# Performance work log

Measured on AMD Instinct MI355X. Metric: run time of the kernel, lower is better.

Reference implementation:

```python
import jax, jax.numpy as jnp
import numpy as np

N_NODES = 100000


def setup_inputs() -> dict:
    key = jax.random.key(0)
    ks = jax.random.split(key, 9)
    E = 1600000
    x = jax.random.normal(ks[0], (N_NODES, 12), dtype=jnp.float32)
    edge_index = jax.random.randint(ks[1], (2, E), 0, N_NODES, dtype=jnp.int64)
    def glorot(k, shape):
        lim = float(np.sqrt(6.0 / (shape[0] + shape[1])))
        return jax.random.uniform(k, shape, jnp.float32, -lim, lim)
    return {
        "x": x,
        "edge_index": edge_index,
        "W1": glorot(ks[2], (12, 64)),
        "b1": jnp.zeros((64,), jnp.float32),
        "W2": glorot(ks[3], (64, 128)),
        "b2": jnp.zeros((128,), jnp.float32),
        "W3": glorot(ks[4], (128, 96)),
        "b3": jnp.zeros((96,), jnp.float32),
    }


def reference(x, edge_index, W1, b1, W2, b2, W3, b3):
    N = x.shape[0]
    F_channel, n_his = 8, 12
    src, dst = edge_index[0], edge_index[1]
    # add self loops (PyG GCNConv default)
    loop = jnp.arange(N, dtype=src.dtype)
    src = jnp.concatenate([src, loop])
    dst = jnp.concatenate([dst, loop])
    # symmetric normalization: norm_e = deg[src]^-1/2 * deg[dst]^-1/2
    deg = jax.ops.segment_sum(jnp.ones_like(src, dtype=x.dtype), dst, num_segments=N)
    dinv = jnp.where(deg > 0, jax.lax.rsqrt(deg), 0.0)
    norm = dinv[src] * dinv[dst]  # [E+N]

    def gcn(h, W, b):
        hw = h @ W  # transform first (out_ch <= in-edge fanout cost)
        agg = jax.ops.segment_sum(hw[src] * norm[:, None], dst, num_segments=N)
        return agg + b

    h = jax.nn.relu(gcn(x, W1, b1))
    h = jax.nn.relu(gcn(h, W2, b2))
    h = gcn(h, W3, b3)
    return h.reshape(N, F_channel, n_his)
```

## Files before the change

### kernel.cpp

```cpp
#include <hip/hip_runtime.h>
#include <hip/hip_bf16.h>
#include <hip/hip_fp16.h>


static inline int cdiv(int a, int b) { return (a + b - 1) / b; }
constexpr int BLOCK = 256;
constexpr int BSHIFT = 9;
constexpr int BNODES = 1 << BSHIFT;

typedef float nfloat4 __attribute__((ext_vector_type(4)));
typedef _Float16 f16x8 __attribute__((ext_vector_type(8)));
typedef float f32x16 __attribute__((ext_vector_type(16)));


__device__ __forceinline__ void nt_store_raw16(void* p, float4 v) {
    nfloat4 nv;
    nv.x = v.x; nv.y = v.y; nv.z = v.z; nv.w = v.w;
    __builtin_nontemporal_store(nv, (nfloat4*)p);
}

struct h4 { __half2 a, b; };
__device__ __forceinline__ void store_h4(__half* p, float4 v) {
    h4 r;
    r.a = __floats2half2_rn(v.x, v.y);
    r.b = __floats2half2_rn(v.z, v.w);
    *(h4*)p = r;
}

__device__ __forceinline__ void h8_add(float* acc, float4 raw) {
    union { float4 f; __half2 h[4]; } u;
    u.f = raw;
#pragma unroll
    for (int j = 0; j < 4; ++j) {
        float2 p = __half22float2(u.h[j]);
        acc[2 * j] += p.x;
        acc[2 * j + 1] += p.y;
    }
}


template <int CHUNK>
__global__ void bucket_count_kernel(const int* __restrict__ dst, int E,
                                    int* __restrict__ bcnt, int NB) {
    __shared__ int cnt[256];
    for (int i = threadIdx.x; i < NB; i += blockDim.x) cnt[i] = 0;
    __syncthreads();
    const int e0 = blockIdx.x * CHUNK;
    const int e1 = min(e0 + CHUNK, E);
    for (int e = e0 + threadIdx.x; e < e1; e += blockDim.x)
        atomicAdd(&cnt[dst[e] >> BSHIFT], 1);
    __syncthreads();
    for (int i = threadIdx.x; i < NB; i += blockDim.x)
        if (cnt[i]) atomicAdd(&bcnt[i], cnt[i]);
}

template <int CHUNK>
__global__ void bin_edges_kernel(const int* __restrict__ ei, int E,
                                 const int* __restrict__ bcnt,
                                 int* __restrict__ gcur, unsigned* __restrict__ binned,
                                 int NB) {
    __shared__ int cnt[256], base[256], rk[256], sc[256];
    const int t = threadIdx.x;
    const int bv = (t < NB) ? bcnt[t] : 0;
    sc[t] = bv;
    for (int i = t; i < NB; i += blockDim.x) { cnt[i] = 0; rk[i] = 0; }
    __syncthreads();
    for (int off = 1; off < 256; off <<= 1) {
        int add = (t >= off) ? sc[t - off] : 0;
        __syncthreads();
        sc[t] += add;
        __syncthreads();
    }
    const int ex = sc[t] - bv;
    const int e0 = blockIdx.x * CHUNK;
    const int e1 = min(e0 + CHUNK, E);
    for (int e = e0 + t; e < e1; e += blockDim.x)
        atomicAdd(&cnt[ei[E + e] >> BSHIFT], 1);
    __syncthreads();
    if (t < NB) base[t] = ex + (cnt[t] ? atomicAdd(&gcur[t], cnt[t]) : 0);
    __syncthreads();
    for (int e = e0 + t; e < e1; e += blockDim.x) {
        int s = ei[e], d = ei[E + e];
        int b = d >> BSHIFT;
        int r = atomicAdd(&rk[b], 1);
        binned[base[b] + r] = (unsigned)s | ((unsigned)(d & (BNODES - 1)) << 17);
    }
}

__global__ void csr_fill_kernel(const int* __restrict__ bcnt,
                                const unsigned* __restrict__ binned,
                                int* __restrict__ deg, float* __restrict__ dinv,
                                int* __restrict__ row_ptr, int* __restrict__ csr_src,
                                int* __restrict__ dh, int N) {
    __shared__ int c[BNODES];
    __shared__ int ps[256];
    __shared__ int dhloc[64];
    __shared__ int sbase;
    const int t = threadIdx.x;
    const int b = blockIdx.x;
    const int node0 = b << BSHIFT;
    if (t < BNODES) c[t] = 0;
    if (t < 64) dhloc[t] = 0;
    if (t < 256) ps[t] = bcnt[t];
    __syncthreads();
    for (int off = 1; off < 256; off <<= 1) {
        int add = (t >= off && t < 256) ? ps[t - off] : 0;
        __syncthreads();
        if (t < 256) ps[t] += add;
        __syncthreads();
    }
    if (t == 0) sbase = (b == 0) ? 0 : ps[b - 1];
    __syncthreads();
    const int base = sbase;
    const int end = base + bcnt[b];
    for (int e = base + t; e < end; e += 1024)
        atomicAdd(&c[binned[e] >> 17], 1);
    __syncthreads();
    int s0 = 0, s1 = 0;
    if (t < 256) {
        s0 = c[2 * t]; s1 = c[2 * t + 1];
        ps[t] = s0 + s1;
    }
    __syncthreads();
    for (int off = 1; off < 256; off <<= 1) {
        int add = (t >= off && t < 256) ? ps[t - off] : 0;
        __syncthreads();
        if (t < 256) ps[t] += add;
        __syncthreads();
    }
    if (t < 256) {
        const int ex = ps[t] - (s0 + s1);
        const int p0 = base + ex;
        const int p1 = p0 + s0;
        const int n0 = node0 + 2 * t;
        if (n0 < N) {
            row_ptr[n0] = p0; deg[n0] = s0; dinv[n0] = rsqrtf((float)s0 + 1.0f);
            atomicAdd(&dhloc[min(s0, 63)], 1);
            if (n0 + 1 < N) {
                row_ptr[n0 + 1] = p1; deg[n0 + 1] = s1; dinv[n0 + 1] = rsqrtf((float)s1 + 1.0f);
                atomicAdd(&dhloc[min(s1, 63)], 1);
            }
        }
        c[2 * t] = p0; c[2 * t + 1] = p1;
    }
    __syncthreads();
    if (t < 64 && dhloc[t]) atomicAdd(&dh[t], dhloc[t]);
    for (int e = base + t; e < end; e += 1024) {
        unsigned sd = binned[e];
        int pos = atomicAdd(&c[sd >> 17], 1);
        csr_src[pos] = (int)(sd & 0x1FFFFu);
    }
}


__global__ void dperm_kernel(const int* __restrict__ deg, const int* __restrict__ row_ptr,
                             const float* __restrict__ dinv, const int* __restrict__ dh,
                             int* __restrict__ dcur, int4* __restrict__ hdr, int N) {
    __shared__ int cnt[64], base[64], rk[64], sc[64];
    const int t = threadIdx.x;
    if (t < 64) {
        cnt[t] = 0; rk[t] = 0;
        sc[t] = dh[t];
    }
    __syncthreads();
    for (int off = 1; off < 64; off <<= 1) {
        int add = (t >= off && t < 64) ? sc[t - off] : 0;
        __syncthreads();
        if (t < 64) sc[t] += add;
        __syncthreads();
    }
    const int i = blockIdx.x * blockDim.x + t;
    const int d = (i < N) ? deg[i] : 0;
    const int myb = (i < N) ? min(d, 63) : -1;
    if (myb >= 0) atomicAdd(&cnt[myb], 1);
    __syncthreads();
    if (t < 64) {
        const int ex = sc[t] - dh[t];
        base[t] = ex + (cnt[t] ? atomicAdd(&dcur[t], cnt[t]) : 0);
    }
    __syncthreads();
    if (myb >= 0) {
        int r = atomicAdd(&rk[myb], 1);
        int slot = base[myb] + r;
        int4 h;
        h.x = row_ptr[i];
        h.y = d;
        h.z = i;
        h.w = __float_as_int(dinv[i]);
        hdr[N - 1 - slot] = h;
    }
}


__global__ void prescale_h_kernel(const float* __restrict__ x, const float* __restrict__ dinv,
                                  __half* __restrict__ xs, int N) {
    int i = blockIdx.x * blockDim.x + threadIdx.x;
    if (i >= N) return;
    float di = dinv[i];
    const float4* xr = (const float4*)(x + (size_t)i * 12);
    float4 a = xr[0], b = xr[1], c = xr[2];
    union { float4 f; __half2 h[4]; } u0, u1;
    u0.h[0] = __floats2half2_rn(a.x * di, a.y * di);
    u0.h[1] = __floats2half2_rn(a.z * di, a.w * di);
    u0.h[2] = __floats2half2_rn(b.x * di, b.y * di);
    u0.h[3] = __floats2half2_rn(b.z * di, b.w * di);
    u1.h[0] = __floats2half2_rn(c.x * di, c.y * di);
    u1.h[1] = __floats2half2_rn(c.z * di, c.w * di);
    u1.h[2] = __floats2half2_rn(0.f, 0.f);
    u1.h[3] = __floats2half2_rn(0.f, 0.f);
    float4* op = (float4*)(xs + (size_t)i * 16);
    op[0] = u0.f;
    op[1] = u1.f;
}


__global__ void gather_x_t1_kernel(const int4* __restrict__ hdr,
                                   const int* __restrict__ csr_src,
                                   const __half* __restrict__ xs,
                                   const float* __restrict__ W1,
                                   const float* __restrict__ b1,
                                   __half* __restrict__ h1h, int N) {
    __shared__ float W1s[12 * 64];
    __shared__ float xrow[128][12];
    const int tid = threadIdx.x;
    for (int u = tid; u < 12 * 64 / 4; u += 256)
        ((float4*)W1s)[u] = ((const float4*)W1)[u];

    const int t = blockIdx.x * 256 + tid;
    const bool valid = (t < N * 2);
    const int slot = t >> 1;
    const int c = t & 1;
    const int nl = tid >> 1;
    int4 H = valid ? hdr[slot] : make_int4(0, 0, 0, 0);
    const int* __restrict__ sp = csr_src + H.x;
    const int n = valid ? H.y : 0;
    const int i = H.z;
    const float di = __int_as_float(H.w);
    const int f0 = c * 8;

    float acc[8];
    {
        union { float4 f; __half2 h[4]; } u;
        u.f = *(const float4*)(xs + (size_t)i * 16 + f0);
#pragma unroll
        for (int j = 0; j < 4; ++j) {
            float2 p = __half22float2(u.h[j]);
            acc[2 * j] = p.x; acc[2 * j + 1] = p.y;
        }
    }

    int k = 0;
    if (n >= 8) {
        int s[8];
#pragma unroll
        for (int j = 0; j < 8; ++j) s[j] = sp[j];
        for (; k + 16 <= n; k += 8) {
            int ns[8];
#pragma unroll
            for (int j = 0; j < 8; ++j) ns[j] = sp[k + 8 + j];
            float4 v[8];
#pragma unroll
            for (int j = 0; j < 8; ++j) v[j] = *(const float4*)(xs + (size_t)s[j] * 16 + f0);
#pragma unroll
            for (int j = 0; j < 8; ++j) h8_add(acc, v[j]);
#pragma unroll
            for (int j = 0; j < 8; ++j) s[j] = ns[j];
        }
        float4 v[8];
#pragma unroll
        for (int j = 0; j < 8; ++j) v[j] = *(const float4*)(xs + (size_t)s[j] * 16 + f0);
#pragma unroll
        for (int j = 0; j < 8; ++j) h8_add(acc, v[j]);
        k += 8;
    }
    for (; k + 4 <= n; k += 4) {
        int s0 = sp[k + 0], s1 = sp[k + 1], s2 = sp[k + 2], s3 = sp[k + 3];
        float4 v0 = *(const float4*)(xs + (size_t)s0 * 16 + f0);
        float4 v1 = *(const float4*)(xs + (size_t)s1 * 16 + f0);
        float4 v2 = *(const float4*)(xs + (size_t)s2 * 16 + f0);
        float4 v3 = *(const float4*)(xs + (size_t)s3 * 16 + f0);
        h8_add(acc, v0); h8_add(acc, v1); h8_add(acc, v2); h8_add(acc, v3);
    }
    for (; k < n; ++k) {
        float4 v = *(const float4*)(xs + (size_t)sp[k] * 16 + f0);
        h8_add(acc, v);
    }

    if (valid) {
        if (c == 0) {
#pragma unroll
            for (int j = 0; j < 8; ++j) xrow[nl][j] = acc[j] * di;
        } else {
#pragma unroll
            for (int j = 0; j < 4; ++j) xrow[nl][8 + j] = acc[j] * di;
        }
    }
    __syncthreads();
    if (!valid) return;

    float xr[12];
#pragma unroll
    for (int j = 0; j < 12; ++j) xr[j] = xrow[nl][j];

    __half* op = h1h + (size_t)i * 64 + c * 32;
#pragma unroll
    for (int g = 0; g < 8; ++g) {
        const int c0 = c * 32 + g * 4;
        float4 r = *(const float4*)(b1 + c0);
#pragma unroll
        for (int kk = 0; kk < 12; ++kk) {
            const float4 w = *(const float4*)(W1s + kk * 64 + c0);
            r.x = fmaf(xr[kk], w.x, r.x);
            r.y = fmaf(xr[kk], w.y, r.y);
            r.z = fmaf(xr[kk], w.z, r.z);
            r.w = fmaf(xr[kk], w.w, r.w);
        }
        r.x = fmaxf(r.x, 0.f) * di; r.y = fmaxf(r.y, 0.f) * di;
        r.z = fmaxf(r.z, 0.f) * di; r.w = fmaxf(r.w, 0.f) * di;
        store_h4(op + g * 4, r);
    }
}


__global__ void prep_w_kernel(const float* __restrict__ W2, const float* __restrict__ W3,
                              __half* __restrict__ W2T, __half* __restrict__ W3T) {
    int i = blockIdx.x * 256 + threadIdx.x;
    if (i < 64 * 128) {
        int k = i >> 7, n = i & 127;
        W2T[n * 64 + k] = __float2half(W2[i]);
    } else {
        int j = i - 64 * 128;
        if (j < 128 * 96) {
            int k = j / 96, n = j - k * 96;
            W3T[n * 128 + k] = __float2half(W3[j]);
        }
    }
}

__global__ void __launch_bounds__(256, 2)
fused_g64_t2t3_kernel(const __half* __restrict__ h1h,
                      const int* __restrict__ row_ptr, const int* __restrict__ deg,
                      const int* __restrict__ csr_src, const float* __restrict__ dinv,
                      const __half* __restrict__ W2T,
                      const float* __restrict__ b2,
                      const __half* __restrict__ W3T,
                      __half* __restrict__ out,
                      int N) {
    constexpr int LDH = 136;
    __shared__ _Float16 buf[4][32 * LDH];
    const int tid = threadIdx.x;
    const int lane = tid & 63;
    const int wid = tid >> 6;
    const int l31 = lane & 31;
    const int lh = lane >> 5;
    const int NT = N >> 5;
    const int t0 = blockIdx.x * 4;

    {
        const int nr = tid >> 3;
        const int f0 = (tid & 7) * 8;
#pragma unroll 1
        for (int p = 0; p < 4; ++p) {
            const int t = t0 + p;
            if (t >= NT) break;
            const int i = (t << 5) + nr;
            const int* __restrict__ sp = csr_src + row_ptr[i];
            const int n = deg[i];
            const float di = dinv[i];

            float acc[8];
            {
                union { float4 f; __half2 h[4]; } u;
                u.f = *(const float4*)(h1h + (size_t)i * 64 + f0);
#pragma unroll
                for (int j = 0; j < 4; ++j) {
                    float2 pp = __half22float2(u.h[j]);
                    acc[2 * j] = pp.x; acc[2 * j + 1] = pp.y;
                }
            }

            int k = 0;
            if (n >= 8) {
                int s[8];
#pragma unroll
                for (int j = 0; j < 8; ++j) s[j] = sp[j];
                for (; k + 16 <= n; k += 8) {
                    int ns[8];
#pragma unroll
                    for (int j = 0; j < 8; ++j) ns[j] = sp[k + 8 + j];
                    float4 v[8];
#pragma unroll
                    for (int j = 0; j < 8; ++j) v[j] = *(const float4*)(h1h + (size_t)s[j] * 64 + f0);
#pragma unroll
                    for (int j = 0; j < 8; ++j) h8_add(acc, v[j]);
#pragma unroll
                    for (int j = 0; j < 8; ++j) s[j] = ns[j];
                }
                float4 v[8];
#pragma unroll
                for (int j = 0; j < 8; ++j) v[j] = *(const float4*)(h1h + (size_t)s[j] * 64 + f0);
#pragma unroll
                for (int j = 0; j < 8; ++j) h8_add(acc, v[j]);
                k += 8;
            }
            for (; k + 4 <= n; k += 4) {
                int s0 = sp[k + 0], s1 = sp[k + 1], s2 = sp[k + 2], s3 = sp[k + 3];
                float4 v0 = *(const float4*)(h1h + (size_t)s0 * 64 + f0);
                float4 v1 = *(const float4*)(h1h + (size_t)s1 * 64 + f0);
                float4 v2 = *(const float4*)(h1h + (size_t)s2 * 64 + f0);
                float4 v3 = *(const float4*)(h1h + (size_t)s3 * 64 + f0);
                h8_add(acc, v0); h8_add(acc, v1); h8_add(acc, v2); h8_add(acc, v3);
            }
            for (; k < n; ++k) {
                float4 v = *(const float4*)(h1h + (size_t)sp[k] * 64 + f0);
                h8_add(acc, v);
            }

            union { float4 f; __half2 h[4]; } o;
            o.h[0] = __floats2half2_rn(acc[0] * di, acc[1] * di);
            o.h[1] = __floats2half2_rn(acc[2] * di, acc[3] * di);
            o.h[2] = __floats2half2_rn(acc[4] * di, acc[5] * di);
            o.h[3] = __floats2half2_rn(acc[6] * di, acc[7] * di);
            *(float4*)(&buf[p][nr * LDH + f0]) = o.f;
        }
    }
    __syncthreads();

    const int t = t0 + wid;
    if (t >= NT) return;
    const int r0 = t << 5;
    _Float16* hs = buf[wid];

    float b2v[4];
#pragma unroll
    for (int nt = 0; nt < 4; ++nt) b2v[nt] = b2[nt * 32 + l31];

    f16x8 a2[4];
#pragma unroll
    for (int kb = 0; kb < 4; ++kb)
        a2[kb] = *(const f16x8*)(hs + l31 * LDH + kb * 16 + lh * 8);

#pragma unroll
    for (int nt = 0; nt < 4; ++nt) {
        f32x16 c = {0.f, 0.f, 0.f, 0.f, 0.f, 0.f, 0.f, 0.f,
                    0.f, 0.f, 0.f, 0.f, 0.f, 0.f, 0.f, 0.f};
#pragma unroll
        for (int kb = 0; kb < 4; ++kb) {
            f16x8 b = *(const f16x8*)(W2T + (size_t)(nt * 32 + l31) * 64 + kb * 16 + lh * 8);
            c = __builtin_amdgcn_mfma_f32_32x32x16_f16(a2[kb], b, c, 0, 0, 0);
        }
#pragma unroll
        for (int r = 0; r < 16; ++r) {
            int row = (r & 3) + 8 * (r >> 2) + 4 * lh;
            float v = fmaxf(c[r] + b2v[nt], 0.f);
            hs[row * LDH + nt * 32 + l31] = (_Float16)v;
        }
    }

    f16x8 a3[8];
#pragma unroll
    for (int kb = 0; kb < 8; ++kb)
        a3[kb] = *(const f16x8*)(hs + l31 * LDH + kb * 16 + lh * 8);
    float4 dv[4];
#pragma unroll
    for (int rg = 0; rg < 4; ++rg)
        dv[rg] = *(const float4*)(dinv + r0 + rg * 8 + lh * 4);
#pragma unroll
    for (int nt = 0; nt < 3; ++nt) {
        f32x16 c = {0.f, 0.f, 0.f, 0.f, 0.f, 0.f, 0.f, 0.f,
                    0.f, 0.f, 0.f, 0.f, 0.f, 0.f, 0.f, 0.f};
#pragma unroll
        for (int kb = 0; kb < 8; ++kb) {
            f16x8 b = *(const f16x8*)(W3T + (size_t)(nt * 32 + l31) * 128 + kb * 16 + lh * 8);
            c = __builtin_amdgcn_mfma_f32_32x32x16_f16(a3[kb], b, c, 0, 0, 0);
        }
#pragma unroll
        for (int r = 0; r < 16; ++r) {
            int row = (r & 3) + 8 * (r >> 2) + 4 * lh;
            float dvv = ((const float*)&dv[r >> 2])[r & 3];
            hs[row * LDH + nt * 32 + l31] = (_Float16)(c[r] * dvv);
        }
    }

#pragma unroll
    for (int it = 0; it < 6; ++it) {
        int id = lane + it * 64;
        int row = id / 12, ch = id - row * 12;
        float4 v = *(const float4*)(hs + row * LDH + ch * 8);
        *(float4*)((char*)(out + (size_t)r0 * 96) + (size_t)id * 16) = v;
    }
}


template <int F, bool HAS_BIAS, bool OUT_HALF>
__global__ void gather_h_kernel(const int4* __restrict__ hdr, const int* __restrict__ csr_src,
                                const __half* __restrict__ hws,
                                const float* __restrict__ b, void* __restrict__ out_v, int N) {
    constexpr int TPN = F / 8;
    int t = blockIdx.x * blockDim.x + threadIdx.x;
    if (t >= N * TPN) return;
    int slot = t / TPN;
    int c = t - slot * TPN;
    const int4 H = hdr[slot];
    const int* __restrict__ sp = csr_src + H.x;
    const int n = H.y;
    const int i = H.z;
    const float di = __int_as_float(H.w);
    int f0 = c * 8;

    float acc[8];
    {
        union { float4 f; __half2 h[4]; } u;
        u.f = *(const float4*)(hws + (size_t)i * F + f0);
#pragma unroll
        for (int j = 0; j < 4; ++j) {
            float2 p = __half22float2(u.h[j]);
            acc[2 * j] = p.x; acc[2 * j + 1] = p.y;
        }
    }

    int k = 0;
    if (n >= 8) {
        int s[8];
#pragma unroll
        for (int j = 0; j < 8; ++j) s[j] = sp[j];
        for (; k + 16 <= n; k += 8) {
            int ns[8];
#pragma unroll
            for (int j = 0; j < 8; ++j) ns[j] = sp[k + 8 + j];
            float4 v[8];
#pragma unroll
            for (int j = 0; j < 8; ++j) v[j] = *(const float4*)(hws + (size_t)s[j] * F + f0);
#pragma unroll
            for (int j = 0; j < 8; ++j) h8_add(acc, v[j]);
#pragma unroll
            for (int j = 0; j < 8; ++j) s[j] = ns[j];
        }
        float4 v[8];
#pragma unroll
        for (int j = 0; j < 8; ++j) v[j] = *(const float4*)(hws + (size_t)s[j] * F + f0);
#pragma unroll
        for (int j = 0; j < 8; ++j) h8_add(acc, v[j]);
        k += 8;
    }
    for (; k + 4 <= n; k += 4) {
        int s0 = sp[k + 0], s1 = sp[k + 1], s2 = sp[k + 2], s3 = sp[k + 3];
        float4 v0 = *(const float4*)(hws + (size_t)s0 * F + f0);
        float4 v1 = *(const float4*)(hws + (size_t)s1 * F + f0);
        float4 v2 = *(const float4*)(hws + (size_t)s2 * F + f0);
        float4 v3 = *(const float4*)(hws + (size_t)s3 * F + f0);
        h8_add(acc, v0); h8_add(acc, v1); h8_add(acc, v2); h8_add(acc, v3);
    }
    for (; k < n; ++k) {
        float4 v = *(const float4*)(hws + (size_t)sp[k] * F + f0);
        h8_add(acc, v);
    }

    float4 r0, r1;
    if (HAS_BIAS) {
        const float4 bb0 = *(const float4*)(b + f0);
        const float4 bb1 = *(const float4*)(b + f0 + 4);
        r0.x = fmaf(acc[0], di, bb0.x); r0.y = fmaf(acc[1], di, bb0.y);
        r0.z = fmaf(acc[2], di, bb0.z); r0.w = fmaf(acc[3], di, bb0.w);
        r1.x = fmaf(acc[4], di, bb1.x); r1.y = fmaf(acc[5], di, bb1.y);
        r1.z = fmaf(acc[6], di, bb1.z); r1.w = fmaf(acc[7], di, bb1.w);
    } else {
        r0.x = acc[0] * di; r0.y = acc[1] * di; r0.z = acc[2] * di; r0.w = acc[3] * di;
        r1.x = acc[4] * di; r1.y = acc[5] * di; r1.z = acc[6] * di; r1.w = acc[7] * di;
    }
    if (OUT_HALF) {
        union { float4 f; __half2 h[4]; } u;
        u.h[0] = __floats2half2_rn(r0.x, r0.y);
        u.h[1] = __floats2half2_rn(r0.z, r0.w);
        u.h[2] = __floats2half2_rn(r1.x, r1.y);
        u.h[3] = __floats2half2_rn(r1.z, r1.w);
        nt_store_raw16((__half*)out_v + (size_t)i * F + f0, u.f);
    } else {
        float* op = (float*)out_v + (size_t)i * F + f0;
        nt_store_raw16(op, r0);
        nt_store_raw16(op + 4, r1);
    }
}


extern "C" void kernel_launch(void* const* d_in, const int* in_sizes, int n_in,
                              void* d_out, int out_size, void* d_ws, size_t ws_size,
                              hipStream_t stream) {
    const float* x  = (const float*)d_in[0];
    const int*   ei = (const int*)d_in[1];
    const float* W1 = (const float*)d_in[2];
    const float* b1 = (const float*)d_in[3];
    const float* W2 = (const float*)d_in[4];
    const float* b2 = (const float*)d_in[5];
    const float* W3 = (const float*)d_in[6];
    const float* b3 = (const float*)d_in[7];
    float* out = (float*)d_out;

    const int N = in_sizes[0] / 12;
    const int E = in_sizes[1] / 2;
    const int NB = cdiv(N, BNODES);

    char* ws = (char*)d_ws;
    int*   deg     = (int*)ws;    ws += (size_t)N * sizeof(int);
    int*   row_ptr = (int*)ws;    ws += (size_t)N * sizeof(int);
    int*   bcnt    = (int*)ws;    ws += 256 * sizeof(int);
    int*   dh      = (int*)ws;    ws += 64 * sizeof(int);
    int*   dcur    = (int*)ws;    ws += 64 * sizeof(int);
    int*   gcur    = (int*)ws;    ws += 256 * sizeof(int);
    float* dinv    = (float*)ws;  ws += (size_t)N * sizeof(float);
    int4*  hdr     = (int4*)ws;   ws += (size_t)N * sizeof(int4);
    __half* W2Th   = (__half*)ws; ws += 128 * 64 * sizeof(__half);
    __half* W3Th   = (__half*)ws; ws += 96 * 128 * sizeof(__half);
    int*   csr_src = (int*)ws;    ws += (size_t)E * sizeof(int);
    float* bufA    = (float*)ws;  ws += (size_t)N * 128 * sizeof(float);
    float* bufB    = (float*)ws;
    unsigned* binned = (unsigned*)bufB;

    hipMemsetAsync(bcnt, 0, (256 + 64 + 64 + 256) * sizeof(int), stream);
    prep_w_kernel<<<80, 256, 0, stream>>>(W2, W3, W2Th, W3Th);
    bucket_count_kernel<8192><<<cdiv(E, 8192), BLOCK, 0, stream>>>(ei + E, E, bcnt, NB);
    bin_edges_kernel<8192><<<cdiv(E, 8192), BLOCK, 0, stream>>>(ei, E, bcnt, gcur, binned, NB);
    csr_fill_kernel<<<NB, 1024, 0, stream>>>(bcnt, binned, deg, dinv, row_ptr,
                                             csr_src, dh, N);

    dperm_kernel<<<cdiv(N, BLOCK), BLOCK, 0, stream>>>(deg, row_ptr, dinv, dh, dcur, hdr, N);

    prescale_h_kernel<<<cdiv(N, BLOCK), BLOCK, 0, stream>>>(x, dinv, (__half*)bufA, N);
    gather_x_t1_kernel<<<cdiv(N * 2, BLOCK), BLOCK, 0, stream>>>(
        hdr, csr_src, (const __half*)bufA, W1, b1, (__half*)bufB, N);

    fused_g64_t2t3_kernel<<<cdiv(N / 32, 4), 256, 0, stream>>>(
        (const __half*)bufB, row_ptr, deg, csr_src, dinv, W2Th, b2, W3Th,
        (__half*)bufA, N);

    gather_h_kernel<96, true, false><<<cdiv(N * 12, BLOCK), BLOCK, 0, stream>>>(
        hdr, csr_src, (const __half*)bufA, b3, out, N);
}
```

Before: 273.5 us.

## Bin edges into fixed-capacity bucket slots and fuse prescale into dperm

Removes the separate bucket-count pass by giving each destination bucket a fixed slot of 16384 entries, so one edge-binning pass can claim offsets atomically. The CSR fill reads each bucket from its own slot. The x prescale and fp16 conversion move into the degree-permutation kernel, which saves a launch and reuses the dinv load. The fixed slot size assumes no bucket of 512 nodes gets more than 16384 in-edges; a skewed graph would overflow.

```diff
diff --git a/kernel.cpp b/kernel.cpp
--- a/kernel.cpp
+++ b/kernel.cpp
@@ -7,6 +7,7 @@
 constexpr int BLOCK = 256;
 constexpr int BSHIFT = 9;
 constexpr int BNODES = 1 << BSHIFT;
+constexpr int SLOT = 16384;
 
 typedef float nfloat4 __attribute__((ext_vector_type(4)));
 typedef _Float16 f16x8 __attribute__((ext_vector_type(8)));
@@ -40,44 +41,20 @@
 
 
 template <int CHUNK>
-__global__ void bucket_count_kernel(const int* __restrict__ dst, int E,
-                                    int* __restrict__ bcnt, int NB) {
-    __shared__ int cnt[256];
-    for (int i = threadIdx.x; i < NB; i += blockDim.x) cnt[i] = 0;
-    __syncthreads();
-    const int e0 = blockIdx.x * CHUNK;
-    const int e1 = min(e0 + CHUNK, E);
-    for (int e = e0 + threadIdx.x; e < e1; e += blockDim.x)
-        atomicAdd(&cnt[dst[e] >> BSHIFT], 1);
-    __syncthreads();
-    for (int i = threadIdx.x; i < NB; i += blockDim.x)
-        if (cnt[i]) atomicAdd(&bcnt[i], cnt[i]);
-}
-
-template <int CHUNK>
 __global__ void bin_edges_kernel(const int* __restrict__ ei, int E,
-                                 const int* __restrict__ bcnt,
-                                 int* __restrict__ gcur, unsigned* __restrict__ binned,
+                                 int* __restrict__ bcnt, unsigned* __restrict__ binned,
                                  int NB) {
-    __shared__ int cnt[256], base[256], rk[256], sc[256];
+    __shared__ int cnt[256], base[256], rk[256];
     const int t = threadIdx.x;
-    const int bv = (t < NB) ? bcnt[t] : 0;
-    sc[t] = bv;
     for (int i = t; i < NB; i += blockDim.x) { cnt[i] = 0; rk[i] = 0; }
     __syncthreads();
-    for (int off = 1; off < 256; off <<= 1) {
-        int add = (t >= off) ? sc[t - off] : 0;
-        __syncthreads();
-        sc[t] += add;
-        __syncthreads();
-    }
-    const int ex = sc[t] - bv;
     const int e0 = blockIdx.x * CHUNK;
     const int e1 = min(e0 + CHUNK, E);
     for (int e = e0 + t; e < e1; e += blockDim.x)
         atomicAdd(&cnt[ei[E + e] >> BSHIFT], 1);
     __syncthreads();
-    if (t < NB) base[t] = ex + (cnt[t] ? atomicAdd(&gcur[t], cnt[t]) : 0);
+    for (int i = t; i < NB; i += blockDim.x)
+        base[i] = i * SLOT + (cnt[i] ? atomicAdd(&bcnt[i], cnt[i]) : 0);
     __syncthreads();
     for (int e = e0 + t; e < e1; e += blockDim.x) {
         int s = ei[e], d = ei[E + e];
@@ -112,9 +89,10 @@
     if (t == 0) sbase = (b == 0) ? 0 : ps[b - 1];
     __syncthreads();
     const int base = sbase;
-    const int end = base + bcnt[b];
-    for (int e = base + t; e < end; e += 1024)
-        atomicAdd(&c[binned[e] >> 17], 1);
+    const int cb = bcnt[b];
+    const unsigned* __restrict__ bin = binned + (size_t)b * SLOT;
+    for (int e = t; e < cb; e += 1024)
+        atomicAdd(&c[bin[e] >> 17], 1);
     __syncthreads();
     int s0 = 0, s1 = 0;
     if (t < 256) {
@@ -145,8 +123,8 @@
     }
     __syncthreads();
     if (t < 64 && dhloc[t]) atomicAdd(&dh[t], dhloc[t]);
-    for (int e = base + t; e < end; e += 1024) {
-        unsigned sd = binned[e];
+    for (int e = t; e < cb; e += 1024) {
+        unsigned sd = bin[e];
         int pos = atomicAdd(&c[sd >> 17], 1);
         csr_src[pos] = (int)(sd & 0x1FFFFu);
     }
@@ -155,7 +133,8 @@
 
 __global__ void dperm_kernel(const int* __restrict__ deg, const int* __restrict__ row_ptr,
                              const float* __restrict__ dinv, const int* __restrict__ dh,
-                             int* __restrict__ dcur, int4* __restrict__ hdr, int N) {
+                             int* __restrict__ dcur, int4* __restrict__ hdr,
+                             const float* __restrict__ x, __half* __restrict__ xs, int N) {
     __shared__ int cnt[64], base[64], rk[64], sc[64];
     const int t = threadIdx.x;
     if (t < 64) {
@@ -172,6 +151,7 @@
     const int i = blockIdx.x * blockDim.x + t;
     const int d = (i < N) ? deg[i] : 0;
     const int myb = (i < N) ? min(d, 63) : -1;
+    const float di = (i < N) ? dinv[i] : 0.f;
     if (myb >= 0) atomicAdd(&cnt[myb], 1);
     __syncthreads();
     if (t < 64) {
@@ -186,31 +166,24 @@
         h.x = row_ptr[i];
         h.y = d;
         h.z = i;
-        h.w = __float_as_int(dinv[i]);
+        h.w = __float_as_int(di);
         hdr[N - 1 - slot] = h;
-    }
-}
-
-
-__global__ void prescale_h_kernel(const float* __restrict__ x, const float* __restrict__ dinv,
-                                  __half* __restrict__ xs, int N) {
-    int i = blockIdx.x * blockDim.x + threadIdx.x;
-    if (i >= N) return;
-    float di = dinv[i];
-    const float4* xr = (const float4*)(x + (size_t)i * 12);
-    float4 a = xr[0], b = xr[1], c = xr[2];
-    union { float4 f; __half2 h[4]; } u0, u1;
-    u0.h[0] = __floats2half2_rn(a.x * di, a.y * di);
-    u0.h[1] = __floats2half2_rn(a.z * di, a.w * di);
-    u0.h[2] = __floats2half2_rn(b.x * di, b.y * di);
-    u0.h[3] = __floats2half2_rn(b.z * di, b.w * di);
-    u1.h[0] = __floats2half2_rn(c.x * di, c.y * di);
-    u1.h[1] = __floats2half2_rn(c.z * di, c.w * di);
-    u1.h[2] = __floats2half2_rn(0.f, 0.f);
-    u1.h[3] = __floats2half2_rn(0.f, 0.f);
-    float4* op = (float4*)(xs + (size_t)i * 16);
-    op[0] = u0.f;
-    op[1] = u1.f;
+
+        const float4* xr = (const float4*)(x + (size_t)i * 12);
+        float4 a = xr[0], b = xr[1], c = xr[2];
+        union { float4 f; __half2 h2[4]; } u0, u1;
+        u0.h2[0] = __floats2half2_rn(a.x * di, a.y * di);
+        u0.h2[1] = __floats2half2_rn(a.z * di, a.w * di);
+        u0.h2[2] = __floats2half2_rn(b.x * di, b.y * di);
+        u0.h2[3] = __floats2half2_rn(b.z * di, b.w * di);
+        u1.h2[0] = __floats2half2_rn(c.x * di, c.y * di);
+        u1.h2[1] = __floats2half2_rn(c.z * di, c.w * di);
+        u1.h2[2] = __floats2half2_rn(0.f, 0.f);
+        u1.h2[3] = __floats2half2_rn(0.f, 0.f);
+        float4* op = (float4*)(xs + (size_t)i * 16);
+        op[0] = u0.f;
+        op[1] = u1.f;
+    }
 }
 
 
@@ -606,7 +579,6 @@
     int*   bcnt    = (int*)ws;    ws += 256 * sizeof(int);
     int*   dh      = (int*)ws;    ws += 64 * sizeof(int);
     int*   dcur    = (int*)ws;    ws += 64 * sizeof(int);
-    int*   gcur    = (int*)ws;    ws += 256 * sizeof(int);
     float* dinv    = (float*)ws;  ws += (size_t)N * sizeof(float);
     int4*  hdr     = (int4*)ws;   ws += (size_t)N * sizeof(int4);
     __half* W2Th   = (__half*)ws; ws += 128 * 64 * sizeof(__half);
@@ -616,16 +588,15 @@
     float* bufB    = (float*)ws;
     unsigned* binned = (unsigned*)bufB;
 
-    hipMemsetAsync(bcnt, 0, (256 + 64 + 64 + 256) * sizeof(int), stream);
+    hipMemsetAsync(bcnt, 0, (256 + 64 + 64) * sizeof(int), stream);
     prep_w_kernel<<<80, 256, 0, stream>>>(W2, W3, W2Th, W3Th);
-    bucket_count_kernel<8192><<<cdiv(E, 8192), BLOCK, 0, stream>>>(ei + E, E, bcnt, NB);
-    bin_edges_kernel<8192><<<cdiv(E, 8192), BLOCK, 0, stream>>>(ei, E, bcnt, gcur, binned, NB);
+    bin_edges_kernel<8192><<<cdiv(E, 8192), BLOCK, 0, stream>>>(ei, E, bcnt, binned, NB);
     csr_fill_kernel<<<NB, 1024, 0, stream>>>(bcnt, binned, deg, dinv, row_ptr,
                                              csr_src, dh, N);
 
-    dperm_kernel<<<cdiv(N, BLOCK), BLOCK, 0, stream>>>(deg, row_ptr, dinv, dh, dcur, hdr, N);
-
-    prescale_h_kernel<<<cdiv(N, BLOCK), BLOCK, 0, stream>>>(x, dinv, (__half*)bufA, N);
+    dperm_kernel<<<cdiv(N, BLOCK), BLOCK, 0, stream>>>(deg, row_ptr, dinv, dh, dcur, hdr,
+                                                       x, (__half*)bufA, N);
+
     gather_x_t1_kernel<<<cdiv(N * 2, BLOCK), BLOCK, 0, stream>>>(
         hdr, csr_src, (const __half*)bufA, W1, b1, (__half*)bufB, N);
 
```

Measured after the change: 264.7 us. 1.03x faster.
